# Optimization experiments

Measured on AMD Instinct MI355X. Metric: run time of the kernel, lower is better.

The kernel has to match this reference:

```python
import jax, jax.numpy as jnp
import numpy as np

B, C, H, W = 64, 512, 32, 32
N, K = 4, 1024          # num_codebooks, num_embeddings
D = C // N              # dims per codebook = 128


def setup_inputs() -> dict:
    key = jax.random.key(0)
    k1, k2 = jax.random.split(key)
    x = jax.random.normal(k1, (B, C, H, W), dtype=jnp.float32)
    embed = jax.random.normal(k2, (N, D, K), dtype=jnp.float32)  # codebooks
    return {"x": x, "embed": embed}


def reference(x, embed):
    """QLayer.up with downsample==1: identity encoder -> multi-codebook VQ.
    Returns (z_q [B,C,H,W], diff scalar, argmin [B,N,H,W], ppl scalar)."""
    P = B * H * W
    # channels-last, split channels into N codebooks of D dims each
    z = jnp.transpose(x, (0, 2, 3, 1)).reshape(P, N, D)          # [P,N,D]
    # squared L2 distance: ||z||^2 - 2 z.e + ||e||^2   -> [P,N,K]
    dist = (jnp.sum(z * z, axis=-1, keepdims=True)
            - 2.0 * jnp.einsum('pnd,ndk->pnk', z, embed)
            + jnp.sum(embed * embed, axis=1)[None])
    idx = jnp.argmin(dist, axis=-1)                              # [P,N] int
    # gather nearest codewords: embed_t [N,K,D]
    embed_t = jnp.transpose(embed, (0, 2, 1))
    q = embed_t[jnp.arange(N)[None, :], idx]                     # [P,N,D]
    q = q.reshape(B, H, W, C)
    z_bhwc = jnp.transpose(x, (0, 2, 3, 1))
    # commitment term and straight-through estimator
    diff = jnp.mean(jnp.square(jax.lax.stop_gradient(q) - z_bhwc))
    z_q = z_bhwc + jax.lax.stop_gradient(q - z_bhwc)
    z_q = jnp.transpose(z_q, (0, 3, 1, 2))                       # [B,C,H,W]
    # perplexity of codebook usage (mean over codebooks)
    counts = jnp.zeros((N, K), jnp.float32).at[
        jnp.broadcast_to(jnp.arange(N)[None, :], idx.shape), idx].add(1.0)
    probs = counts / P
    ppl = jnp.mean(jnp.exp(-jnp.sum(probs * jnp.log(probs + 1e-10), axis=-1)))
    argmin = jnp.transpose(idx.reshape(B, H, W, N), (0, 3, 1, 2))  # [B,N,H,W]
    return z_q, diff, argmin, ppl
```

## Files before the change

kernel.cpp:

```cpp
#include <hip/hip_runtime.h>
#include <math.h>

#define BB  64
#define CC  512
#define NN  4
#define KK  1024
#define DD  128
#define HW  1024
#define PP  65536

#define OFF_DIFF 33554432UL
#define OFF_ARG  33554433UL
#define OFF_PPL  33816577UL

#define WS_HIST   0
#define WS_DSUM   16384
#define WS_WLCNT  16392
#define WS_ENORM  16416
#define WS_EBF    32800
#define WS_EMBT   (32800 + 128*8192)
#define WS_WL     (WS_EMBT + NN*KK*DD*4)

#define DELTA 0.0625f

typedef _Float16 half8 __attribute__((ext_vector_type(8)));
typedef float f32x4 __attribute__((ext_vector_type(4)));

#define MFMA16(a, b, c) __builtin_amdgcn_mfma_f32_16x16x32_f16(a, b, c, 0, 0, 0)

__device__ __forceinline__ int swz(int row, int dbyte) {
    return (row * 256 + dbyte) ^ ((row & 15) << 4);
}
__device__ __forceinline__ void gl2lds16(const void* g, void* l) {
    __builtin_amdgcn_global_load_lds(
        (const __attribute__((address_space(1))) unsigned int*)g,
        (__attribute__((address_space(3))) unsigned int*)l, 16, 0, 0);
}

__global__ __launch_bounds__(256) void vq_prep(const float* __restrict__ embed,
                                               char* __restrict__ ebf,
                                               float* __restrict__ embt,
                                               float* __restrict__ enorm,
                                               unsigned* __restrict__ hist,
                                               double* __restrict__ dsum,
                                               unsigned* __restrict__ wlcnt) {
    __shared__ float sred[16][16];
    const int e = blockIdx.x;
    const int n = e >> 6, kt16 = e & 63, k0 = kt16 * 16;
    const int t = threadIdx.x, kr = t & 15, dc = t >> 4;
    if (t < 16) hist[e * 16 + t] = 0u;
    if (e == 0 && t == 0) { *dsum = 0.0; *wlcnt = 0u; }

    const float* src = embed + ((size_t)n * DD + dc * 8) * KK + k0 + kr;
    char* tile = ebf + ((size_t)(n * 32 + (kt16 >> 1))) * 8192;
    const int row = (kt16 & 1) * 16 + kr;
    float fv[8];
    #pragma unroll
    for (int r = 0; r < 8; ++r) fv[r] = src[(size_t)r * KK];
    float s = 0.f;
    half8 vh;
    #pragma unroll
    for (int r = 0; r < 8; ++r) {
        vh[r] = (_Float16)fv[r];
        s = fmaf(fv[r], fv[r], s);
    }
    *(half8*)(tile + swz(row, dc * 16)) = vh;
    {
        float* drow = embt + ((size_t)n * KK + k0 + kr) * DD + dc * 8;
        *(float4*)(drow)     = make_float4(fv[0], fv[1], fv[2], fv[3]);
        *(float4*)(drow + 4) = make_float4(fv[4], fv[5], fv[6], fv[7]);
    }
    sred[dc][kr] = s;
    __syncthreads();
    if (t < 16) {
        float a = 0.f;
        #pragma unroll
        for (int d2 = 0; d2 < 16; ++d2) a += sred[d2][t];
        enorm[n * KK + k0 + t] = -0.5f * a;
    }
}

#define TOP2(C0, C1, MF, KP)                                                  \
    _Pragma("unroll")                                                         \
    for (int i_ = 0; i_ < 4; ++i_) {                                          \
        float v_ = C0[i_] + C1[i_];                                           \
        int r_ = (MF) * 4 + i_;                                               \
        float mn_ = fminf(pb1[r_], v_);                                       \
        pb2[r_] = fmaxf(pb2[r_], mn_);                                        \
        pk1[r_] = (v_ > pb1[r_]) ? (KP) : pk1[r_];                            \
        pb1[r_] = fmaxf(pb1[r_], v_);                                         \
    }

#define VSTEP(ACW, ACR, KTL, KPREV)                                           \
  {                                                                           \
    if (gW < 128) {                                                           \
        const char* s_ = ebf + (size_t)gW * 8192 + t * 16;                    \
        char* d_ = ebase + (bufW << 13) + t * 16;                             \
        gl2lds16(s_, d_);                                                     \
        gl2lds16(s_ + 4096, d_ + 4096);                                       \
    }                                                                         \
    ++gW; bufW = (bufW == 5) ? 0 : bufW + 1;                                  \
    const int rb_ = bufR << 13;                                               \
    bufR = (bufR == 5) ? 0 : bufR + 1;                                        \
    half8 bh0 = *(const half8*)(ebase + rb_ + bo0);                           \
    half8 bh1 = *(const half8*)(ebase + rb_ + bo1);                           \
    half8 bh2 = *(const half8*)(ebase + rb_ + bo2);                           \
    half8 bh3 = *(const half8*)(ebase + rb_ + bo3);                           \
    float e2a = enls[((KTL) << 5) + koff];                                    \
    f32x4 e2v = {e2a, e2a, e2a, e2a};                                         \
    __builtin_amdgcn_s_setprio(1);                                            \
    ACW##00 = MFMA16(af[0][0], bh0, e2v);                                     \
    ACW##00 = MFMA16(af[0][1], bh1, ACW##00);                                 \
    ACW##01 = MFMA16(af[0][2], bh2, zz4);                                     \
    ACW##01 = MFMA16(af[0][3], bh3, ACW##01);                                 \
    ACW##10 = MFMA16(af[1][0], bh0, e2v);                                     \
    ACW##10 = MFMA16(af[1][1], bh1, ACW##10);                                 \
    ACW##11 = MFMA16(af[1][2], bh2, zz4);                                     \
    ACW##11 = MFMA16(af[1][3], bh3, ACW##11);                                 \
    __builtin_amdgcn_s_setprio(0);                                            \
    TOP2(ACR##00, ACR##01, 0, KPREV);                                         \
    TOP2(ACR##10, ACR##11, 1, KPREV);                                         \
  }

__global__ __launch_bounds__(256, 2) void vq_main(const float* __restrict__ x,
                                                  const char* __restrict__ ebf,
                                                  const float* __restrict__ embt,
                                                  const float* __restrict__ enormg,
                                                  float* __restrict__ out,
                                                  unsigned* __restrict__ hist,
                                                  double* __restrict__ dsum,
                                                  unsigned* __restrict__ wlcnt,
                                                  int2* __restrict__ wl, int wlcap) {
    __shared__ __attribute__((aligned(16))) _Float16 zs[64 * 128];
    __shared__ __attribute__((aligned(16))) char ebuf[6][8192];
    __shared__ __attribute__((aligned(16))) float enls[KK];
    __shared__ int   idx_s[NN][64];
    __shared__ float red_b1[2][64], red_b2[2][64];
    __shared__ int   red_k1[2][64];
    __shared__ float wsum[4];

    const int t   = threadIdx.x;
    const int blk = blockIdx.x;
    const int b   = blk >> 4;
    const int hw0 = (blk & 15) << 6;
    const int w  = t >> 6, l = t & 63;
    const int pq = w >> 1;
    const int ks = w & 1;
    const int tk = l & 15, lg = l >> 4;
    const int koff = ks * 16 + tk;

    char* ebase = (char*)&ebuf[0][0];
    const int bo0 = swz(koff, (0 * 32 + lg * 8) * 2);
    const int bo1 = swz(koff, (1 * 32 + lg * 8) * 2);
    const int bo2 = swz(koff, (2 * 32 + lg * 8) * 2);
    const int bo3 = swz(koff, (3 * 32 + lg * 8) * 2);

    const f32x4 zz4 = {0.f, 0.f, 0.f, 0.f};
    const f32x4 m1e30 = {-1e30f, -1e30f, -1e30f, -1e30f};

    int bufR = 0, bufW = 4, gW = 4;
    float znacc = 0.f, sumb1 = 0.f;

    for (int n = 0; n < NN; ++n) {
        __syncthreads();
        gl2lds16((const char*)(enormg + n * KK) + t * 16, (char*)enls + t * 16);
        if (n == 0) {
            #pragma unroll
            for (int j = 0; j < 4; ++j) {
                const char* s_ = ebf + (size_t)j * 8192 + t * 16;
                char* d_ = ebase + j * 8192 + t * 16;
                gl2lds16(s_, d_);
                gl2lds16(s_ + 4096, d_ + 4096);
            }
        }
        {
            const int p = t & 63, dchunk = t >> 6;
            const float* xp = x + ((size_t)b * CC + n * DD + dchunk * 32) * HW + hw0 + p;
            float fv[32];
            #pragma unroll
            for (int r = 0; r < 32; ++r) fv[r] = xp[(size_t)r * HW];
            #pragma unroll
            for (int j = 0; j < 4; ++j) {
                half8 vh;
                #pragma unroll
                for (int r = 0; r < 8; ++r) {
                    float f = fv[j * 8 + r];
                    vh[r] = (_Float16)f;
                    znacc = fmaf(f, f, znacc);
                }
                *(half8*)((char*)zs + swz(p, (dchunk * 32 + j * 8) * 2)) = vh;
            }
        }
        __syncthreads();

        half8 af[2][4];
        #pragma unroll
        for (int mf = 0; mf < 2; ++mf)
            #pragma unroll
            for (int ds = 0; ds < 4; ++ds)
                af[mf][ds] = *(const half8*)((const char*)zs +
                               swz(pq * 32 + mf * 16 + tk, (ds * 32 + lg * 8) * 2));

        float pb1[8], pb2[8]; int pk1[8];
        #pragma unroll
        for (int r = 0; r < 8; ++r) { pb1[r] = -INFINITY; pb2[r] = -INFINITY; pk1[r] = 0; }

        f32x4 accA00, accA01, accA10, accA11;
        f32x4 accB00 = m1e30, accB01 = m1e30, accB10 = m1e30, accB11 = m1e30;

        #pragma unroll 1
        for (int wnd = 0; wnd < 16; ++wnd) {
            if (n == NN - 1 && wnd == 15)
                asm volatile("s_waitcnt vmcnt(0)" ::: "memory");
            else
                asm volatile("s_waitcnt vmcnt(4)" ::: "memory");
            __builtin_amdgcn_s_barrier();
            __builtin_amdgcn_sched_barrier(0);
            const int ka = wnd * 2;
            VSTEP(accA, accB, ka,     ((ka - 1) << 5) + koff)
            VSTEP(accB, accA, ka + 1, (ka << 5) + koff)
        }
        TOP2(accB00, accB01, 0, (31 << 5) + koff);
        TOP2(accB10, accB11, 1, (31 << 5) + koff);

        #pragma unroll
        for (int off = 1; off < 16; off <<= 1) {
            #pragma unroll
            for (int r = 0; r < 8; ++r) {
                float ob1 = __shfl_xor(pb1[r], off);
                float ob2 = __shfl_xor(pb2[r], off);
                int   ok1 = __shfl_xor(pk1[r], off);
                float nb2 = fmaxf(pb2[r], ob2);
                if (ob1 > pb1[r] || (ob1 == pb1[r] && ok1 < pk1[r])) {
                    pb2[r] = fmaxf(nb2, pb1[r]); pb1[r] = ob1; pk1[r] = ok1;
                } else {
                    pb2[r] = fmaxf(nb2, ob1);
                }
            }
        }
        if (tk == 0) {
            #pragma unroll
            for (int mf = 0; mf < 2; ++mf)
                #pragma unroll
                for (int i = 0; i < 4; ++i) {
                    int p = pq * 32 + mf * 16 + lg * 4 + i, r = mf * 4 + i;
                    red_b1[ks][p] = pb1[r]; red_b2[ks][p] = pb2[r]; red_k1[ks][p] = pk1[r];
                }
        }
        __syncthreads();
        if (t < 64) {
            int p = t;
            float m1 = red_b1[0][p], m2 = red_b2[0][p]; int mk = red_k1[0][p];
            {
                float ob1 = red_b1[1][p], ob2 = red_b2[1][p]; int ok = red_k1[1][p];
                float nb2 = fmaxf(m2, ob2);
                if (ob1 > m1 || (ob1 == m1 && ok < mk)) { m2 = fmaxf(nb2, m1); m1 = ob1; mk = ok; }
                else                                    { m2 = fmaxf(nb2, ob1); }
            }
            idx_s[n][p] = mk;
            atomicAdd(&hist[n * KK + mk], 1u);
            sumb1 += m1;
            if ((m1 - m2) < DELTA * 0.5f) {
                unsigned pos = atomicAdd(wlcnt, 1u);
                if ((int)pos < wlcap) wl[pos] = make_int2(b * HW + hw0 + p, n);
            }
        }
    }

    {
        float tot = znacc - 2.f * sumb1;
        #pragma unroll
        for (int off = 32; off > 0; off >>= 1) tot += __shfl_down(tot, off);
        if (l == 0) wsum[w] = tot;
        __syncthreads();
        if (t == 0) {
            double sd = 0.0;
            #pragma unroll
            for (int ww = 0; ww < 4; ++ww) sd += (double)wsum[ww];
            atomicAdd(dsum, sd);
        }
    }

    {
        int n2 = t >> 6, p = t & 63;
        out[OFF_ARG + (size_t)b * (NN * HW) + (size_t)n2 * HW + hw0 + p] = (float)idx_s[n2][p];
    }

    {
        const int p = t & 63, dchunk = t >> 6;
        #pragma unroll
        for (int n2 = 0; n2 < NN; ++n2) {
            int k = idx_s[n2][p];
            const float4* src = (const float4*)(embt + ((size_t)n2 * KK + k) * DD + dchunk * 32);
            const int c0 = n2 * 128 + dchunk * 32;
            #pragma unroll
            for (int r = 0; r < 8; ++r) {
                float4 q = src[r];
                out[((size_t)b * CC + c0 + r * 4 + 0) * HW + hw0 + p] = q.x;
                out[((size_t)b * CC + c0 + r * 4 + 1) * HW + hw0 + p] = q.y;
                out[((size_t)b * CC + c0 + r * 4 + 2) * HW + hw0 + p] = q.z;
                out[((size_t)b * CC + c0 + r * 4 + 3) * HW + hw0 + p] = q.w;
            }
        }
    }
}

#define ACCQ(U, V, J)                                                         \
  { double a0_ = (double)(V).x, a1_ = (double)(V).y,                          \
           a2_ = (double)(V).z, a3_ = (double)(V).w;                          \
    U = fma(a0_, zd2[(J)*4+0] - a0_, U);                                      \
    U = fma(a1_, zd2[(J)*4+1] - a1_, U);                                      \
    U = fma(a2_, zd2[(J)*4+2] - a2_, U);                                      \
    U = fma(a3_, zd2[(J)*4+3] - a3_, U); }

__global__ __launch_bounds__(256) void vq_refine(const float* __restrict__ x,
                                                 const float* __restrict__ embt,
                                                 float* __restrict__ out,
                                                 unsigned* __restrict__ hist,
                                                 const unsigned* __restrict__ wlcnt,
                                                 const int2* __restrict__ wl, int wlcap) {
    __shared__ float  zrow[DD];
    __shared__ double wbest[4];
    __shared__ int    wbestk[4];
    __shared__ int    flip_s;
    const int t = threadIdx.x;
    const int w = t >> 6, l = t & 63;
    const int rlane = l >> 3;
    const int dseg  = l & 7;

    unsigned wc = *wlcnt;
    int nitems = (int)(wc < (unsigned)wlcap ? wc : (unsigned)wlcap);

    for (int it = blockIdx.x; it < nitems; it += gridDim.x) {
        __syncthreads();
        int2 item = wl[it];
        int p = item.x, n = item.y;
        int b = p >> 10, hw = p & 1023;

        if (t < DD) zrow[t] = x[((size_t)b * CC + n * DD + t) * HW + hw];
        __syncthreads();

        double zd2[16];
        #pragma unroll
        for (int i = 0; i < 16; ++i) zd2[i] = 2.0 * (double)zrow[dseg * 16 + i];

        const float* en = embt + (size_t)n * KK * DD;
        double best = -INFINITY; int bestk = 0;
        const int rbase = w * 256;

        #pragma unroll 1
        for (int g0 = 0; g0 < 32; g0 += 2) {
            const int rowA = rbase + g0 * 8 + rlane;
            const int rowB = rowA + 8;
            const float4* erA = (const float4*)(en + (size_t)rowA * DD + dseg * 16);
            const float4* erB = (const float4*)(en + (size_t)rowB * DD + dseg * 16);
            float4 va0 = erA[0], va1 = erA[1], va2 = erA[2], va3 = erA[3];
            float4 vb0 = erB[0], vb1 = erB[1], vb2 = erB[2], vb3 = erB[3];
            double uA = 0.0, uB = 0.0;
            ACCQ(uA, va0, 0) ACCQ(uA, va1, 1) ACCQ(uA, va2, 2) ACCQ(uA, va3, 3)
            ACCQ(uB, vb0, 0) ACCQ(uB, vb1, 1) ACCQ(uB, vb2, 2) ACCQ(uB, vb3, 3)
            uA += __shfl_xor(uA, 1); uB += __shfl_xor(uB, 1);
            uA += __shfl_xor(uA, 2); uB += __shfl_xor(uB, 2);
            uA += __shfl_xor(uA, 4); uB += __shfl_xor(uB, 4);
            if (uA > best) { best = uA; bestk = rowA; }
            if (uB > best) { best = uB; bestk = rowB; }
        }
        #pragma unroll
        for (int mask = 8; mask <= 32; mask <<= 1) {
            double ob = __shfl_xor(best, mask);
            int    ok = __shfl_xor(bestk, mask);
            if (ob > best || (ob == best && ok < bestk)) { best = ob; bestk = ok; }
        }
        if (l == 0) { wbest[w] = best; wbestk[w] = bestk; }
        __syncthreads();
        if (t == 0) {
            double m = wbest[0]; int mk = wbestk[0];
            #pragma unroll
            for (int ww = 1; ww < 4; ++ww)
                if (wbest[ww] > m) { m = wbest[ww]; mk = wbestk[ww]; }
            size_t slot = OFF_ARG + (size_t)b * (NN * HW) + (size_t)n * HW + hw;
            int oldk = (int)out[slot];
            flip_s = -1;
            if (mk != oldk) {
                out[slot] = (float)mk;
                atomicSub(&hist[n * KK + oldk], 1u);
                atomicAdd(&hist[n * KK + mk], 1u);
                flip_s = mk;
            }
        }
        __syncthreads();
        int fk = flip_s;
        if (fk >= 0 && t < DD)
            out[((size_t)b * CC + n * DD + t) * HW + hw] = en[(size_t)fk * DD + t];
    }
}

__global__ __launch_bounds__(256) void vq_final(const unsigned* __restrict__ hist,
                                                const double* __restrict__ dsum,
                                                float* __restrict__ out) {
    __shared__ double red[256];
    __shared__ double hn[NN];
    const int t = threadIdx.x;
    for (int n = 0; n < NN; ++n) {
        double acc = 0.0;
        for (int k = t; k < KK; k += 256) {
            double pr = (double)hist[n * KK + k] / (double)PP;
            acc += pr * log(pr + 1e-10);
        }
        red[t] = acc;
        __syncthreads();
        for (int off = 128; off > 0; off >>= 1) {
            if (t < off) red[t] += red[t + off];
            __syncthreads();
        }
        if (t == 0) hn[n] = red[0];
        __syncthreads();
    }
    if (t == 0) {
        double ppl = 0.0;
        for (int n = 0; n < NN; ++n) ppl += exp(-hn[n]);
        out[OFF_PPL]  = (float)(ppl * 0.25);
        out[OFF_DIFF] = (float)(*dsum / (double)((size_t)BB * CC * HW));
    }
}

extern "C" void kernel_launch(void* const* d_in, const int* in_sizes, int n_in,
                              void* d_out, int out_size, void* d_ws, size_t ws_size,
                              hipStream_t stream) {
    const float* x     = (const float*)d_in[0];
    const float* embed = (const float*)d_in[1];
    float* out = (float*)d_out;
    char*  ws  = (char*)d_ws;

    unsigned* hist   = (unsigned*)(ws + WS_HIST);
    double*   dsum   = (double*)  (ws + WS_DSUM);
    unsigned* wlcnt  = (unsigned*)(ws + WS_WLCNT);
    float*    enorm  = (float*)   (ws + WS_ENORM);
    char*     ebf    = ws + WS_EBF;
    float*    embt   = (float*)   (ws + WS_EMBT);
    int2*     wl     = (int2*)    (ws + WS_WL);

    long long cap = ((long long)ws_size - WS_WL) / (long long)sizeof(int2);
    int wlcap = cap < 0 ? 0 : (cap > 65536 ? 65536 : (int)cap);

    vq_prep  <<<256,  256, 0, stream>>>(embed, ebf, embt, enorm, hist, dsum, wlcnt);
    vq_main  <<<1024, 256, 0, stream>>>(x, ebf, embt, enorm, out, hist, dsum, wlcnt, wl, wlcap);
    vq_refine<<<2048, 256, 0, stream>>>(x, embt, out, hist, wlcnt, wl, wlcap);
    vq_final <<<1,    256, 0, stream>>>(hist, dsum, out);
}
```

Baseline: 316.1 us.

## Write z_q and argmin per codebook inside loop with paired float2 stores

Moves the argmin output and the gather-and-write of quantized codewords into the per-codebook loop, so each codebook's output is written right after its argmin. The goal is to overlap global stores with the next codebook's MFMA work and to shrink the index buffer to a single codebook. Each thread now handles two adjacent pixels and writes float2 values, which widens the stores. The cost is an extra __syncthreads per codebook. Any refine pass that later rewrites outputs still runs after this kernel.

```diff
diff --git a/kernel.cpp b/kernel.cpp
--- a/kernel.cpp
+++ b/kernel.cpp
@@ -134,7 +134,7 @@
     __shared__ __attribute__((aligned(16))) _Float16 zs[64 * 128];
     __shared__ __attribute__((aligned(16))) char ebuf[6][8192];
     __shared__ __attribute__((aligned(16))) float enls[KK];
-    __shared__ int   idx_s[NN][64];
+    __shared__ int   idx_s[64];
     __shared__ float red_b1[2][64], red_b2[2][64];
     __shared__ int   red_k1[2][64];
     __shared__ float wsum[4];
@@ -257,13 +257,33 @@
                 if (ob1 > m1 || (ob1 == m1 && ok < mk)) { m2 = fmaxf(nb2, m1); m1 = ob1; mk = ok; }
                 else                                    { m2 = fmaxf(nb2, ob1); }
             }
-            idx_s[n][p] = mk;
+            idx_s[p] = mk;
             atomicAdd(&hist[n * KK + mk], 1u);
             sumb1 += m1;
             if ((m1 - m2) < DELTA * 0.5f) {
                 unsigned pos = atomicAdd(wlcnt, 1u);
                 if ((int)pos < wlcap) wl[pos] = make_int2(b * HW + hw0 + p, n);
             }
+            out[OFF_ARG + (size_t)b * (NN * HW) + (size_t)n * HW + hw0 + p] = (float)mk;
+        }
+        __syncthreads();
+
+        {
+            const int pp = (t & 31) * 2, cc8 = t >> 5;
+            const int ka = idx_s[pp], kb = idx_s[pp + 1];
+            const float4* ra = (const float4*)(embt + ((size_t)n * KK + ka) * DD + cc8 * 16);
+            const float4* rb = (const float4*)(embt + ((size_t)n * KK + kb) * DD + cc8 * 16);
+            float4 qa0 = ra[0], qa1 = ra[1], qa2 = ra[2], qa3 = ra[3];
+            float4 qb0 = rb[0], qb1 = rb[1], qb2 = rb[2], qb3 = rb[3];
+            float qa[16] = {qa0.x,qa0.y,qa0.z,qa0.w, qa1.x,qa1.y,qa1.z,qa1.w,
+                            qa2.x,qa2.y,qa2.z,qa2.w, qa3.x,qa3.y,qa3.z,qa3.w};
+            float qb[16] = {qb0.x,qb0.y,qb0.z,qb0.w, qb1.x,qb1.y,qb1.z,qb1.w,
+                            qb2.x,qb2.y,qb2.z,qb2.w, qb3.x,qb3.y,qb3.z,qb3.w};
+            #pragma unroll
+            for (int j = 0; j < 16; ++j) {
+                *(float2*)&out[((size_t)b * CC + n * DD + cc8 * 16 + j) * HW + hw0 + pp]
+                    = make_float2(qa[j], qb[j]);
+            }
         }
     }
 
@@ -278,29 +298,6 @@
             #pragma unroll
             for (int ww = 0; ww < 4; ++ww) sd += (double)wsum[ww];
             atomicAdd(dsum, sd);
-        }
-    }
-
-    {
-        int n2 = t >> 6, p = t & 63;
-        out[OFF_ARG + (size_t)b * (NN * HW) + (size_t)n2 * HW + hw0 + p] = (float)idx_s[n2][p];
-    }
-
-    {
-        const int p = t & 63, dchunk = t >> 6;
-        #pragma unroll
-        for (int n2 = 0; n2 < NN; ++n2) {
-            int k = idx_s[n2][p];
-            const float4* src = (const float4*)(embt + ((size_t)n2 * KK + k) * DD + dchunk * 32);
-            const int c0 = n2 * 128 + dchunk * 32;
-            #pragma unroll
-            for (int r = 0; r < 8; ++r) {
-                float4 q = src[r];
-                out[((size_t)b * CC + c0 + r * 4 + 0) * HW + hw0 + p] = q.x;
-                out[((size_t)b * CC + c0 + r * 4 + 1) * HW + hw0 + p] = q.y;
-                out[((size_t)b * CC + c0 + r * 4 + 2) * HW + hw0 + p] = q.z;
-                out[((size_t)b * CC + c0 + r * 4 + 3) * HW + hw0 + p] = q.w;
-            }
         }
     }
 }
```

New measurement: 321.7 us. Within noise of the previous version (+1.8%).
